# Kernel tuning notes

Hardware: AMD Instinct MI355X
Metric: run time of the kernel (lower is better)

Reference implementation:

```python
import jax, jax.numpy as jnp
import numpy as np

N = 8192
IN_FEATS = 512
OUT_FEATS = 512


def setup_inputs() -> dict:
    key = jax.random.key(0)
    k_adj, k_feat, k_w = jax.random.split(key, 3)
    adj = jax.random.uniform(k_adj, (N, N), dtype=jnp.float32)
    features = jax.random.normal(k_feat, (N, IN_FEATS), dtype=jnp.float32)
    # nn.Linear(in_feats, out_feats, bias=False): weight is [out, in]; we store transposed [in, out]
    W = jax.random.normal(k_w, (IN_FEATS, OUT_FEATS), dtype=jnp.float32) / np.sqrt(IN_FEATS)
    return {"adj": adj, "features": features, "W": W}


def reference(adj, features, W):
    n = adj.shape[0]
    # adj + I (self loops)
    a = adj + jnp.eye(n, dtype=adj.dtype)
    # symmetric degree normalization D^{-1/2} A D^{-1/2}
    deg = jnp.sum(a, axis=1)  # [N]
    d_inv_sqrt = jnp.where(deg > 0, jax.lax.rsqrt(deg), 0.0)  # inf -> 0 as in torch code
    # diag(d) @ a @ diag(d) == d[:,None] * a * d[None,:] (algebraic simplification of O(N^3) diag matmuls)
    norm_adj = d_inv_sqrt[:, None] * a * d_inv_sqrt[None, :]  # [N, N]
    h = norm_adj @ features  # [N, in]
    return h @ W  # [N, out]
```

## Files before the change

kernel.cpp:

```cpp
#include <hip/hip_runtime.h>
#include <cstdint>
#include <cstddef>

#define NN 8192
#define NF 512

typedef __attribute__((ext_vector_type(8))) short bf16x8;
typedef __attribute__((ext_vector_type(4))) float f32x4;

__device__ __forceinline__ unsigned short f2bf_bits(float f) {
  unsigned u = __builtin_bit_cast(unsigned, f);
  u += 0x7FFFu + ((u >> 16) & 1u);
  return (unsigned short)(u >> 16);
}

__device__ __forceinline__ bf16x8 cvt8(float4 a, float4 b) {
  bf16x8 r;
  r[0] = (short)f2bf_bits(a.x); r[1] = (short)f2bf_bits(a.y);
  r[2] = (short)f2bf_bits(a.z); r[3] = (short)f2bf_bits(a.w);
  r[4] = (short)f2bf_bits(b.x); r[5] = (short)f2bf_bits(b.y);
  r[6] = (short)f2bf_bits(b.z); r[7] = (short)f2bf_bits(b.w);
  return r;
}

__device__ __forceinline__ void gld_lds16(const void* g, void* l) {
  __builtin_amdgcn_global_load_lds(
      (const __attribute__((address_space(1))) unsigned int*)g,
      (__attribute__((address_space(3))) unsigned int*)l, 16, 0, 0);
}

template <bool CVT>
__global__ void k_rowsum(const float* __restrict__ adj, float* __restrict__ dinv,
                         short* __restrict__ adjb) {
  const int row = blockIdx.x;
  const float4* p = (const float4*)(adj + (size_t)row * NN);
  short* ob = CVT ? (adjb + (size_t)row * NN) : nullptr;
  float s = 0.f;
#pragma unroll
  for (int j = 0; j < 8; ++j) {
    float4 v = p[j * 256 + threadIdx.x];
    s += (v.x + v.y) + (v.z + v.w);
    if (CVT) {
      ushort4 o;
      o.x = f2bf_bits(v.x); o.y = f2bf_bits(v.y);
      o.z = f2bf_bits(v.z); o.w = f2bf_bits(v.w);
      *(ushort4*)&ob[(size_t)(j * 256 + threadIdx.x) * 4] = o;
    }
  }
#pragma unroll
  for (int off = 32; off > 0; off >>= 1) s += __shfl_down(s, off, 64);
  __shared__ float red[4];
  if ((threadIdx.x & 63) == 0) red[threadIdx.x >> 6] = s;
  __syncthreads();
  if (threadIdx.x == 0) {
    float deg = red[0] + red[1] + red[2] + red[3] + 1.0f;
    dinv[row] = (deg > 0.f) ? (1.0f / sqrtf(deg)) : 0.f;
  }
}

template <bool SCALE>
__global__ void k_transpose(const float* __restrict__ src, int rows, int cols,
                            const float* __restrict__ dinv, short* __restrict__ dst) {
  __shared__ float tile[32][33];
  const int c0 = blockIdx.x * 32, r0 = blockIdx.y * 32;
  const int tx = threadIdx.x & 31, ty = threadIdx.x >> 5;
#pragma unroll
  for (int i = 0; i < 32; i += 8) {
    float v = src[(size_t)(r0 + ty + i) * cols + c0 + tx];
    if (SCALE) v *= dinv[r0 + ty + i];
    tile[ty + i][tx] = v;
  }
  __syncthreads();
#pragma unroll
  for (int i = 0; i < 32; i += 8)
    dst[(size_t)(c0 + ty + i) * rows + r0 + tx] = (short)f2bf_bits(tile[tx][ty + i]);
}

template <bool A_BF16, bool GCN_EPI>
__global__ __launch_bounds__(512, 2)
void k_gemm2(const void* __restrict__ Ap, const short* __restrict__ Bt,
             int N, int K,
             const float* __restrict__ dinv, const float* __restrict__ feat,
             void* __restrict__ Cp) {
  __shared__ __align__(16) short As[4][128 * 64];
  __shared__ __align__(16) short Bs[4][128 * 64];
  const int tid = threadIdx.x;
  const int lane = tid & 63;
  const int w = tid >> 6;
  const int wm = (w >> 1) & 1, wn = w & 1, kk = w >> 2;

  const int bid = blockIdx.y * gridDim.x + blockIdx.x;
  const int nb = gridDim.x * gridDim.y;
  const int sbid = ((nb & 7) == 0) ? ((bid & 7) * (nb >> 3) + (bid >> 3)) : bid;
  const int n0 = (sbid % gridDim.x) * 128;
  const int m0 = (sbid / gridDim.x) * 128;
  const int nt = K >> 6;

  f32x4 acc[4][4];
#pragma unroll
  for (int m = 0; m < 4; ++m)
#pragma unroll
    for (int n = 0; n < 4; ++n) acc[m][n] = (f32x4){0.f, 0.f, 0.f, 0.f};

  const int lr = lane & 15, kg = lane >> 4;
  const int lc = (kk << 2) + kg;

  auto stage_b = [&](int buf, int t) {
    const int kofs = t << 6;
#pragma unroll
    for (int q = 0; q < 2; ++q) {
      const int rblk = (w << 4) + (q << 3);
      const int r = rblk + (lane >> 3);
      const int sc = (lane & 7) ^ (r & 7);
      gld_lds16(Bt + (size_t)(n0 + r) * K + kofs + (sc << 3), &Bs[buf][rblk << 6]);
    }
  };
  auto stage_a = [&](int buf, int t) {
    const int kofs = t << 6;
    const short* Ab = (const short*)Ap;
#pragma unroll
    for (int q = 0; q < 2; ++q) {
      const int rblk = (w << 4) + (q << 3);
      const int r = rblk + (lane >> 3);
      const int sc = (lane & 7) ^ (r & 7);
      gld_lds16(Ab + (size_t)(m0 + r) * K + kofs + (sc << 3), &As[buf][rblk << 6]);
    }
  };
  auto stage_a_f32 = [&](int buf, int t) {
    const int kofs = t << 6;
    const float* Af = (const float*)Ap;
    const int r = tid >> 2;
    const int c0 = (tid & 3) << 4;
    const float* s = Af + (size_t)(m0 + r) * K + kofs + c0;
    float4 x0 = ((const float4*)s)[0], x1 = ((const float4*)s)[1];
    float4 x2 = ((const float4*)s)[2], x3 = ((const float4*)s)[3];
    const int cc = (tid & 3) << 1;
    *(bf16x8*)&As[buf][(r << 6) + ((cc ^ (r & 7)) << 3)]       = cvt8(x0, x1);
    *(bf16x8*)&As[buf][(r << 6) + (((cc + 1) ^ (r & 7)) << 3)] = cvt8(x2, x3);
  };

  auto read_a = [&](int buf, bf16x8* a) {
#pragma unroll
    for (int m = 0; m < 4; ++m) {
      const int r = (wm << 6) + (m << 4) + lr;
      a[m] = *(const bf16x8*)&As[buf][(r << 6) + ((lc ^ (r & 7)) << 3)];
    }
  };
  auto read_b2 = [&](int buf, int nh, bf16x8* b) {
#pragma unroll
    for (int i = 0; i < 2; ++i) {
      const int r = (wn << 6) + (((nh << 1) + i) << 4) + lr;
      b[i] = *(const bf16x8*)&Bs[buf][(r << 6) + ((lc ^ (r & 7)) << 3)];
    }
  };
  auto mfma8 = [&](bf16x8* a, bf16x8* b, int nh) {
#pragma unroll
    for (int m = 0; m < 4; ++m)
#pragma unroll
      for (int i = 0; i < 2; ++i)
        acc[m][(nh << 1) + i] =
            __builtin_amdgcn_mfma_f32_16x16x32_bf16(a[m], b[i], acc[m][(nh << 1) + i], 0, 0, 0);
  };

  if constexpr (A_BF16) {
    stage_a(0, 0); stage_b(0, 0);
    stage_a(1, 1); stage_b(1, 1);
    asm volatile("s_waitcnt vmcnt(4)" ::: "memory");
    __builtin_amdgcn_s_barrier();
    __builtin_amdgcn_sched_barrier(0);

    for (int t = 0; t < nt; ++t) {
      const int cur = t & 3;
      const bool more = (t + 2 < nt);
      bf16x8 a[4], b0[2], b1[2];
      read_a(cur, a);
      read_b2(cur, 0, b0);
      if (more) stage_a((t + 2) & 3, t + 2);
      __builtin_amdgcn_s_barrier();
      asm volatile("s_waitcnt lgkmcnt(0)" ::: "memory");
      __builtin_amdgcn_sched_barrier(0);
      __builtin_amdgcn_s_setprio(1);
      mfma8(a, b0, 0);
      __builtin_amdgcn_s_setprio(0);
      __builtin_amdgcn_sched_barrier(0);
      read_b2(cur, 1, b1);
      if (more) stage_b((t + 2) & 3, t + 2);
      asm volatile("s_waitcnt lgkmcnt(0)" ::: "memory");
      __builtin_amdgcn_sched_barrier(0);
      __builtin_amdgcn_s_setprio(1);
      mfma8(a, b1, 1);
      __builtin_amdgcn_s_setprio(0);
      __builtin_amdgcn_sched_barrier(0);
      if (more)                asm volatile("s_waitcnt vmcnt(4)" ::: "memory");
      else if (t + 1 < nt)     asm volatile("s_waitcnt vmcnt(0)" ::: "memory");
      __builtin_amdgcn_s_barrier();
      __builtin_amdgcn_sched_barrier(0);
    }
  } else {
    stage_a_f32(0, 0); stage_b(0, 0);
    stage_a_f32(1, 1); stage_b(1, 1);
    __syncthreads();
    for (int t = 0; t < nt; ++t) {
      const int cur = t & 3;
      if (t + 2 < nt) { stage_a_f32((t + 2) & 3, t + 2); stage_b((t + 2) & 3, t + 2); }
      bf16x8 a[4], b0[2], b1[2];
      read_a(cur, a); read_b2(cur, 0, b0); read_b2(cur, 1, b1);
      __builtin_amdgcn_s_setprio(1);
      mfma8(a, b0, 0); mfma8(a, b1, 1);
      __builtin_amdgcn_s_setprio(0);
      __syncthreads();
    }
  }

  __syncthreads();
  float* red = (float*)&As[0][0];
  if (w >= 4) {
    float* my = red + ((w - 4) << 12);
#pragma unroll
    for (int m = 0; m < 4; ++m)
#pragma unroll
      for (int n = 0; n < 4; ++n)
        *(f32x4*)&my[(((m << 2) + n) << 8) + (lane << 2)] = acc[m][n];
  }
  __syncthreads();
  if (w < 4) {
    float* my = red + (w << 12);
#pragma unroll
    for (int m = 0; m < 4; ++m)
#pragma unroll
      for (int n = 0; n < 4; ++n)
        acc[m][n] += *(const f32x4*)&my[(((m << 2) + n) << 8) + (lane << 2)];

    const int cl = lane & 15, rg = lane >> 4;
#pragma unroll
    for (int m = 0; m < 4; ++m) {
#pragma unroll
      for (int n = 0; n < 4; ++n) {
#pragma unroll
        for (int j = 0; j < 4; ++j) {
          const int gi = m0 + (wm << 6) + (m << 4) + (rg << 2) + j;
          const int gn = n0 + (wn << 6) + (n << 4) + cl;
          const float v = acc[m][n][j];
          if constexpr (GCN_EPI) {
            const float d = dinv[gi];
            const float hv = d * v + d * d * feat[(size_t)gi * NF + gn];
            ((unsigned short*)Cp)[(size_t)gi * N + gn] = f2bf_bits(hv);
          } else {
            ((float*)Cp)[(size_t)gi * N + gn] = v;
          }
        }
      }
    }
  }
}

extern "C" void kernel_launch(void* const* d_in, const int* in_sizes, int n_in,
                              void* d_out, int out_size, void* d_ws, size_t ws_size,
                              hipStream_t stream) {
  const float* adj  = (const float*)d_in[0];
  const float* feat = (const float*)d_in[1];
  const float* W    = (const float*)d_in[2];

  char* ws = (char*)d_ws;
  float* dinv = (float*)ws;
  short* FbT  = (short*)(ws + 32768);
  short* WbT  = (short*)(ws + 32768 + 8388608);
  short* Hb   = (short*)(ws + 32768 + 8388608 + 524288);
  short* adjb = (short*)(ws + 32768 + 8388608 + 524288 + 8388608);
  float* out  = (float*)d_out;
  const bool big_ws = ws_size >= (size_t)(32768 + 8388608 + 524288 + 8388608) +
                                 (size_t)NN * NN * 2;

  if (big_ws) {
    k_rowsum<true><<<NN, 256, 0, stream>>>(adj, dinv, adjb);
  } else {
    k_rowsum<false><<<NN, 256, 0, stream>>>(adj, dinv, nullptr);
  }
  k_transpose<true ><<<dim3(NF / 32, NN / 32), 256, 0, stream>>>(feat, NN, NF, dinv, FbT);
  k_transpose<false><<<dim3(NF / 32, NF / 32), 256, 0, stream>>>(W, NF, NF, nullptr, WbT);

  if (big_ws) {
    k_gemm2<true, true ><<<dim3(NF / 128, NN / 128), 512, 0, stream>>>(
        adjb, FbT, NF, NN, dinv, feat, Hb);
  } else {
    k_gemm2<false, true ><<<dim3(NF / 128, NN / 128), 512, 0, stream>>>(
        adj, FbT, NF, NN, dinv, feat, Hb);
  }
  k_gemm2<true, false><<<dim3(NF / 128, NN / 128), 512, 0, stream>>>(
      Hb, WbT, NF, NF, nullptr, nullptr, out);
}
```

Before: 205.1 us.

## Split adjacency GEMM along K into partial buffers with separate reduce epilogue

Replaces the fused adjacency×features GEMM with a split-K kernel over four K slices, each writing fp32 partial tiles to workspace. A separate elementwise kernel then sums the partials and applies the degree scaling and self-loop term before storing bf16. This raises the number of blocks to improve CU occupancy, at the cost of extra partial-buffer memory traffic, a simpler non-pipelined main loop, and a larger workspace requirement that may trigger the fallback path.

```diff
diff --git a/kernel.cpp b/kernel.cpp
--- a/kernel.cpp
+++ b/kernel.cpp
@@ -4,6 +4,7 @@
 
 #define NN 8192
 #define NF 512
+#define SPLITK 4
 
 typedef __attribute__((ext_vector_type(8))) short bf16x8;
 typedef __attribute__((ext_vector_type(4))) float f32x4;
@@ -74,6 +75,103 @@
 #pragma unroll
   for (int i = 0; i < 32; i += 8)
     dst[(size_t)(c0 + ty + i) * rows + r0 + tx] = (short)f2bf_bits(tile[tx][ty + i]);
+}
+
+__global__ __launch_bounds__(256, 4)
+void k_gemm3(const short* __restrict__ Ab, const short* __restrict__ Bt,
+             int N, int K, float* __restrict__ Pout) {
+  __shared__ __align__(16) short As[128 * 64];
+  __shared__ __align__(16) short Bs[128 * 64];
+  const int tid = threadIdx.x;
+  const int lane = tid & 63;
+  const int w = tid >> 6;
+  const int wm = w >> 1, wn = w & 1;
+
+  const int bid = blockIdx.y * gridDim.x + blockIdx.x;
+  const int nb = gridDim.x * gridDim.y;
+  const int sbid = ((nb & 7) == 0) ? ((bid & 7) * (nb >> 3) + (bid >> 3)) : bid;
+  const int n0 = (sbid % gridDim.x) * 128;
+  const int m0 = (sbid / gridDim.x) * 128;
+  const int kz = blockIdx.z;
+  const int ksl = K / SPLITK;
+  const int kbase = kz * ksl;
+  const int nt = ksl >> 6;
+  float* Cp = Pout + (size_t)kz * ((size_t)NN * N);
+
+  f32x4 acc[4][4];
+#pragma unroll
+  for (int m = 0; m < 4; ++m)
+#pragma unroll
+    for (int n = 0; n < 4; ++n) acc[m][n] = (f32x4){0.f, 0.f, 0.f, 0.f};
+
+  const int lr = lane & 15, kg = lane >> 4;
+
+  for (int t = 0; t < nt; ++t) {
+    const int kofs = kbase + (t << 6);
+#pragma unroll
+    for (int q = 0; q < 4; ++q) {
+      const int rblk = (w << 5) + (q << 3);
+      const int r = rblk + (lane >> 3);
+      const int sc = (lane & 7) ^ (r & 7);
+      gld_lds16(Ab + (size_t)(m0 + r) * K + kofs + (sc << 3), &As[rblk << 6]);
+      gld_lds16(Bt + (size_t)(n0 + r) * K + kofs + (sc << 3), &Bs[rblk << 6]);
+    }
+    __syncthreads();
+#pragma unroll
+    for (int kk = 0; kk < 2; ++kk) {
+      const int lc = (kk << 2) + kg;
+      bf16x8 a[4], b[4];
+#pragma unroll
+      for (int m = 0; m < 4; ++m) {
+        const int r = (wm << 6) + (m << 4) + lr;
+        a[m] = *(const bf16x8*)&As[(r << 6) + ((lc ^ (r & 7)) << 3)];
+      }
+#pragma unroll
+      for (int n = 0; n < 4; ++n) {
+        const int r = (wn << 6) + (n << 4) + lr;
+        b[n] = *(const bf16x8*)&Bs[(r << 6) + ((lc ^ (r & 7)) << 3)];
+      }
+#pragma unroll
+      for (int m = 0; m < 4; ++m)
+#pragma unroll
+        for (int n = 0; n < 4; ++n)
+          acc[m][n] = __builtin_amdgcn_mfma_f32_16x16x32_bf16(a[m], b[n], acc[m][n], 0, 0, 0);
+    }
+    __syncthreads();
+  }
+
+  const int cl = lane & 15, rg = lane >> 4;
+#pragma unroll
+  for (int m = 0; m < 4; ++m)
+#pragma unroll
+    for (int n = 0; n < 4; ++n)
+#pragma unroll
+      for (int j = 0; j < 4; ++j) {
+        const int gi = m0 + (wm << 6) + (m << 4) + (rg << 2) + j;
+        const int gn = n0 + (wn << 6) + (n << 4) + cl;
+        Cp[(size_t)gi * N + gn] = acc[m][n][j];
+      }
+}
+
+__global__ void k_reduce(const float* __restrict__ P, const float* __restrict__ dinv,
+                         const float* __restrict__ feat, short* __restrict__ Hb) {
+  const size_t idx = ((size_t)blockIdx.x * 256 + threadIdx.x) * 4;
+  const int i = (int)(idx >> 9);
+  const size_t stride = (size_t)NN * NF;
+  float4 s = *(const float4*)&P[idx];
+#pragma unroll
+  for (int kz = 1; kz < SPLITK; ++kz) {
+    float4 p = *(const float4*)&P[kz * stride + idx];
+    s.x += p.x; s.y += p.y; s.z += p.z; s.w += p.w;
+  }
+  const float d = dinv[i], d2 = d * d;
+  float4 f = *(const float4*)&feat[idx];
+  ushort4 o;
+  o.x = f2bf_bits(d * s.x + d2 * f.x);
+  o.y = f2bf_bits(d * s.y + d2 * f.y);
+  o.z = f2bf_bits(d * s.z + d2 * f.z);
+  o.w = f2bf_bits(d * s.w + d2 * f.w);
+  *(ushort4*)&Hb[idx] = o;
 }
 
 template <bool A_BF16, bool GCN_EPI>
@@ -138,7 +236,6 @@
     *(bf16x8*)&As[buf][(r << 6) + ((cc ^ (r & 7)) << 3)]       = cvt8(x0, x1);
     *(bf16x8*)&As[buf][(r << 6) + (((cc + 1) ^ (r & 7)) << 3)] = cvt8(x2, x3);
   };
-
   auto read_a = [&](int buf, bf16x8* a) {
 #pragma unroll
     for (int m = 0; m < 4; ++m) {
@@ -168,7 +265,6 @@
     asm volatile("s_waitcnt vmcnt(4)" ::: "memory");
     __builtin_amdgcn_s_barrier();
     __builtin_amdgcn_sched_barrier(0);
-
     for (int t = 0; t < nt; ++t) {
       const int cur = t & 3;
       const bool more = (t + 2 < nt);
@@ -191,8 +287,8 @@
       mfma8(a, b1, 1);
       __builtin_amdgcn_s_setprio(0);
       __builtin_amdgcn_sched_barrier(0);
-      if (more)                asm volatile("s_waitcnt vmcnt(4)" ::: "memory");
-      else if (t + 1 < nt)     asm volatile("s_waitcnt vmcnt(0)" ::: "memory");
+      if (more)            asm volatile("s_waitcnt vmcnt(4)" ::: "memory");
+      else if (t + 1 < nt) asm volatile("s_waitcnt vmcnt(0)" ::: "memory");
       __builtin_amdgcn_s_barrier();
       __builtin_amdgcn_sched_barrier(0);
     }
@@ -230,12 +326,11 @@
 #pragma unroll
       for (int n = 0; n < 4; ++n)
         acc[m][n] += *(const f32x4*)&my[(((m << 2) + n) << 8) + (lane << 2)];
-
     const int cl = lane & 15, rg = lane >> 4;
 #pragma unroll
-    for (int m = 0; m < 4; ++m) {
-#pragma unroll
-      for (int n = 0; n < 4; ++n) {
+    for (int m = 0; m < 4; ++m)
+#pragma unroll
+      for (int n = 0; n < 4; ++n)
 #pragma unroll
         for (int j = 0; j < 4; ++j) {
           const int gi = m0 + (wm << 6) + (m << 4) + (rg << 2) + j;
@@ -249,8 +344,6 @@
             ((float*)Cp)[(size_t)gi * N + gn] = v;
           }
         }
-      }
-    }
   }
 }
 
@@ -267,9 +360,11 @@
   short* WbT  = (short*)(ws + 32768 + 8388608);
   short* Hb   = (short*)(ws + 32768 + 8388608 + 524288);
   short* adjb = (short*)(ws + 32768 + 8388608 + 524288 + 8388608);
+  float* part = (float*)(ws + 32768 + 8388608 + 524288 + 8388608 + 134217728);
   float* out  = (float*)d_out;
-  const bool big_ws = ws_size >= (size_t)(32768 + 8388608 + 524288 + 8388608) +
-                                 (size_t)NN * NN * 2;
+  const size_t need = (size_t)32768 + 8388608 + 524288 + 8388608 + 134217728 +
+                      (size_t)SPLITK * NN * NF * 4;
+  const bool big_ws = ws_size >= need;
 
   if (big_ws) {
     k_rowsum<true><<<NN, 256, 0, stream>>>(adj, dinv, adjb);
@@ -280,10 +375,10 @@
   k_transpose<false><<<dim3(NF / 32, NF / 32), 256, 0, stream>>>(W, NF, NF, nullptr, WbT);
 
   if (big_ws) {
-    k_gemm2<true, true ><<<dim3(NF / 128, NN / 128), 512, 0, stream>>>(
-        adjb, FbT, NF, NN, dinv, feat, Hb);
+    k_gemm3<<<dim3(NF / 128, NN / 128, SPLITK), 256, 0, stream>>>(adjb, FbT, NF, NN, part);
+    k_reduce<<<(NN * NF) / (256 * 4), 256, 0, stream>>>(part, dinv, feat, Hb);
   } else {
-    k_gemm2<false, true ><<<dim3(NF / 128, NN / 128), 512, 0, stream>>>(
+    k_gemm2<false, true><<<dim3(NF / 128, NN / 128), 512, 0, stream>>>(
         adj, FbT, NF, NN, dinv, feat, Hb);
   }
   k_gemm2<true, false><<<dim3(NF / 128, NN / 128), 512, 0, stream>>>(
```

Result: slower. 217.2 us (+5.9%).
